# Kernel tuning notes

Hardware: AMD Instinct MI355X
Metric: run time of the kernel (lower is better)

The kernel has to match this reference:

```python
import jax, jax.numpy as jnp
import numpy as np

L, D_IN, D_MODEL, N_LAYERS = 4096, 8, 256, 2
ED, N, K = 512, 16, 4          # d_inner = 2*d_model, d_state, d_conv
DT_RANK = 16                   # ceil(d_model/16)
EPS = 1e-5


def setup_inputs() -> dict:
    key = jax.random.key(0)
    ks = jax.random.split(key, 10)
    def g(k, shape, s=0.02):
        return jax.random.normal(k, shape, jnp.float32) * s
    A_init = jnp.tile(jnp.arange(1, N + 1, dtype=jnp.float32), (N_LAYERS, ED, 1))
    return {
        "x": jax.random.normal(ks[0], (L, D_IN), jnp.float32),
        "fc_in_w": g(ks[1], (D_MODEL, D_IN), 0.1),
        "fc_in_b": jnp.zeros((D_MODEL,), jnp.float32),
        "fc_out_w": g(ks[2], (1, D_MODEL), 0.1),
        "fc_out_b": jnp.zeros((1,), jnp.float32),
        "norm_w": jnp.ones((N_LAYERS, D_MODEL), jnp.float32),
        "in_proj_w": g(ks[3], (N_LAYERS, 2 * ED, D_MODEL)),
        "conv_w": g(ks[4], (N_LAYERS, ED, 1, K), 0.1),
        "conv_b": jnp.zeros((N_LAYERS, ED), jnp.float32),
        "x_proj_w": g(ks[5], (N_LAYERS, DT_RANK + 2 * N, ED)),
        "dt_proj_w": g(ks[6], (N_LAYERS, ED, DT_RANK), 0.1),
        "dt_proj_b": jnp.full((N_LAYERS, ED), -4.0, jnp.float32),  # softplus(-4)~0.018
        "A_log": jnp.log(A_init),
        "D": jnp.ones((N_LAYERS, ED), jnp.float32),
        "out_proj_w": g(ks[7], (N_LAYERS, D_MODEL, ED)),
    }


def rmsnorm(x, w):
    return x * jax.lax.rsqrt(jnp.mean(x * x, axis=-1, keepdims=True) + EPS) * w


def causal_depthwise_conv(x, w, b):
    # x: [L, ED], w: [ED, 1, K] -> causal depthwise conv along L
    y = jax.lax.conv_general_dilated(
        x.T[None],  # [1, ED, L]
        w, (1,), [(K - 1, 0)],
        dimension_numbers=("NCH", "OIH", "NCH"),
        feature_group_count=ED)
    return y[0].T + b  # [L, ED]


def mamba_block(x, p):
    norm_w, in_w, cw, cb, xp_w, dtw, dtb, a_log, d, out_w = p
    xn = rmsnorm(x, norm_w)
    xz = xn @ in_w.T                      # [L, 2*ED]
    xi, z = xz[:, :ED], xz[:, ED:]
    xc = jax.nn.silu(causal_depthwise_conv(xi, cw, cb))   # [L, ED]
    dbc = xc @ xp_w.T                     # [L, DT_RANK + 2N]
    delta = jax.nn.softplus(dbc[:, :DT_RANK] @ dtw.T + dtb)  # [L, ED]
    B = dbc[:, DT_RANK:DT_RANK + N]       # [L, N]
    C = dbc[:, DT_RANK + N:]              # [L, N]
    A = -jnp.exp(a_log)                   # [ED, N]
    dA = jnp.exp(delta[:, :, None] * A[None])                 # [L, ED, N]
    dBx = delta[:, :, None] * B[:, None, :] * xc[:, :, None]  # [L, ED, N]

    def step(h, inp):
        da, dbx, c = inp
        h = da * h + dbx                  # [ED, N]
        return h, jnp.einsum("en,n->e", h, c)

    _, ys = jax.lax.scan(step, jnp.zeros((ED, N), x.dtype), (dA, dBx, C))
    y = (ys + d * xc) * jax.nn.silu(z)
    return x + y @ out_w.T


def forward(x, fc_in_w, fc_in_b, fc_out_w, fc_out_b, norm_w, in_proj_w, conv_w,
            conv_b, x_proj_w, dt_proj_w, dt_proj_b, A_log, D, out_proj_w):
    h = x @ fc_in_w.T + fc_in_b           # [L, D_MODEL]

    def layer(h, p):
        return mamba_block(h, p), None

    h, _ = jax.lax.scan(layer, h, (norm_w, in_proj_w, conv_w, conv_b, x_proj_w,
                                   dt_proj_w, dt_proj_b, A_log, D, out_proj_w))
    out = jnp.tanh(h @ fc_out_w.T + fc_out_b)  # [L, 1]
    return out.reshape(-1)


def reference(x, fc_in_w, fc_in_b, fc_out_w, fc_out_b, norm_w, in_proj_w, conv_w,
              conv_b, x_proj_w, dt_proj_w, dt_proj_b, A_log, D, out_proj_w):
    return forward(x, fc_in_w, fc_in_b, fc_out_w, fc_out_b, norm_w, in_proj_w,
                   conv_w, conv_b, x_proj_w, dt_proj_w, dt_proj_b, A_log, D,
                   out_proj_w)
```

## Files before the change

kernel.cpp:

```cpp
#include <hip/hip_runtime.h>
#include <math.h>

#define LSEQ 4096
#define D_IN 8
#define D_MODEL 256
#define ED 512
#define NSTATE 16
#define KCONV 4
#define DT_RANK 16
#define EPS 1e-5f
#define NCHUNK 256
#define CHUNK 16

typedef short short8 __attribute__((ext_vector_type(8)));
typedef unsigned short ushort8 __attribute__((ext_vector_type(8)));
typedef unsigned short ushort4v __attribute__((ext_vector_type(4)));
typedef float f32x4 __attribute__((ext_vector_type(4)));

__device__ __forceinline__ float sigmoidf_(float x){ return 1.f/(1.f+__expf(-x)); }
__device__ __forceinline__ float siluf_(float x){ return x*sigmoidf_(x); }
__device__ __forceinline__ float softplusf_(float x){
  return (x > 20.f) ? x : log1pf(__expf(x));
}
__device__ __forceinline__ unsigned short f2bf(float f){
  unsigned int u = __float_as_uint(f);
  return (unsigned short)((u + 0x7fffu + ((u>>16)&1u)) >> 16);
}
__device__ __forceinline__ float bf2f(unsigned short u){
  return __uint_as_float(((unsigned int)u) << 16);
}

__global__ void k_prep(const float* __restrict__ x, const float* __restrict__ fiw,
                       const float* __restrict__ fib, const float* __restrict__ ipw,
                       const float* __restrict__ xpw, const float* __restrict__ opw,
                       float* __restrict__ h, unsigned short* __restrict__ wip,
                       unsigned short* __restrict__ wxp, unsigned short* __restrict__ wop){
  int b = blockIdx.x, tid = threadIdx.x;
  if (b < 816) {
    int i4 = b*256 + tid;
    const float* src; unsigned short* dst;
    if (i4 < 131072)      { src = ipw; dst = wip; }
    else if (i4 < 143360) { i4 -= 131072; src = xpw; dst = wxp; }
    else                  { i4 -= 143360; src = opw; dst = wop; }
    float4 v = ((const float4*)src)[i4];
    ushort4v o;
    o.x = f2bf(v.x); o.y = f2bf(v.y); o.z = f2bf(v.z); o.w = f2bf(v.w);
    ((ushort4v*)dst)[i4] = o;
  } else {
    int idx = (b-816)*256 + tid;
    int t = idx >> 8, d = idx & 255;
    float acc = fib[d];
#pragma unroll
    for (int i = 0; i < D_IN; ++i) acc += x[t*D_IN+i]*fiw[d*D_IN+i];
    h[idx] = acc;
  }
}

template<int WM, int WN, bool RMS, bool ACC, bool ABF16, bool CBF16>
__global__ __launch_bounds__(256) void k_gemm_mfma(
    const void* __restrict__ Ap, const unsigned short* __restrict__ B,
    void* __restrict__ Cp, int M, int N, int K, const float* __restrict__ nwp)
{
  constexpr int BM = 32*WM, BN = 32*WN, LDT = 72;
  const float* A = (const float*)Ap;
  const unsigned short* Ab = (const unsigned short*)Ap;
  float* Cf = (float*)Cp;
  unsigned short* Cb = (unsigned short*)Cp;
  __shared__ unsigned short As[BM*LDT];
  __shared__ unsigned short Bs[BN*LDT];
  __shared__ float rms_lds[BM];
  __shared__ float nws[D_MODEL];
  const int tid = threadIdx.x;
  const int bm = blockIdx.x*BM, bn = blockIdx.y*BN;
  const int w = tid >> 6, lane = tid & 63;
  const int mb = (w>>1)*WM*16, nb = (w&1)*WN*16;
  const int lr = lane & 15, lk = (lane>>4)*8;
  if (RMS) {
    nws[tid] = nwp[tid];
    constexpr int TPR = 256/BM;
    constexpr int SEG = D_MODEL/TPR;
    int row = tid / TPR, part = tid % TPR;
    const float* ap = A + (size_t)(bm+row)*K + part*SEG;
    float s = 0.f;
#pragma unroll
    for (int i = 0; i < SEG; i += 4) {
      float4 v = *(const float4*)&ap[i];
      s += v.x*v.x + v.y*v.y + v.z*v.z + v.w*v.w;
    }
#pragma unroll
    for (int m = TPR>>1; m; m >>= 1) s += __shfl_xor(s, m);
    if (part == 0) rms_lds[row] = rsqrtf(s*(1.f/D_MODEL) + EPS);
    __syncthreads();
  }
  f32x4 acc[WM][WN] = {};
  for (int k0 = 0; k0 < K; k0 += 64) {
#pragma unroll 2
    for (int s = tid; s < BM*8; s += 256) {
      int row = s>>3, kg = (s&7)*8;
      if (ABF16) {
        *(ushort8*)&As[row*LDT+kg] = *(const ushort8*)&Ab[(size_t)(bm+row)*K + k0 + kg];
      } else {
        const float* ap = &A[(size_t)(bm+row)*K + k0 + kg];
        float4 a0 = *(const float4*)ap, a1 = *(const float4*)(ap+4);
        if (RMS) {
          float rs = rms_lds[row];
          a0.x *= rs*nws[k0+kg+0]; a0.y *= rs*nws[k0+kg+1];
          a0.z *= rs*nws[k0+kg+2]; a0.w *= rs*nws[k0+kg+3];
          a1.x *= rs*nws[k0+kg+4]; a1.y *= rs*nws[k0+kg+5];
          a1.z *= rs*nws[k0+kg+6]; a1.w *= rs*nws[k0+kg+7];
        }
        ushort8 o;
        o[0]=f2bf(a0.x); o[1]=f2bf(a0.y); o[2]=f2bf(a0.z); o[3]=f2bf(a0.w);
        o[4]=f2bf(a1.x); o[5]=f2bf(a1.y); o[6]=f2bf(a1.z); o[7]=f2bf(a1.w);
        *(ushort8*)&As[row*LDT+kg] = o;
      }
    }
#pragma unroll 2
    for (int s = tid; s < BN*8; s += 256) {
      int row = s>>3, kg = (s&7)*8;
      *(ushort8*)&Bs[row*LDT+kg] = *(const ushort8*)&B[(size_t)(bn+row)*K + k0 + kg];
    }
    __syncthreads();
#pragma unroll
    for (int kk = 0; kk < 2; ++kk) {
      short8 af[WM], bfr[WN];
#pragma unroll
      for (int i = 0; i < WM; ++i) af[i]  = *(const short8*)&As[(mb+i*16+lr)*LDT + kk*32 + lk];
#pragma unroll
      for (int j = 0; j < WN; ++j) bfr[j] = *(const short8*)&Bs[(nb+j*16+lr)*LDT + kk*32 + lk];
#pragma unroll
      for (int i = 0; i < WM; ++i)
#pragma unroll
        for (int j = 0; j < WN; ++j)
          acc[i][j] = __builtin_amdgcn_mfma_f32_16x16x32_bf16(af[i], bfr[j], acc[i][j], 0, 0, 0);
    }
    __syncthreads();
  }
#pragma unroll
  for (int i = 0; i < WM; ++i)
#pragma unroll
    for (int j = 0; j < WN; ++j) {
      int col = bn + nb + j*16 + lr;
#pragma unroll
      for (int r = 0; r < 4; ++r) {
        int row = bm + mb + i*16 + (lane>>4)*4 + r;
        size_t o = (size_t)row*N + col;
        if (CBF16)      Cb[o] = f2bf(acc[i][j][r]);
        else if (ACC)   Cf[o] = Cf[o] + acc[i][j][r];
        else            Cf[o] = acc[i][j][r];
      }
    }
}

__global__ __launch_bounds__(512) void k_cxps1(
    const unsigned short* __restrict__ xzb, const float* __restrict__ cw,
    const float* __restrict__ cb, const unsigned short* __restrict__ wxp,
    const float* __restrict__ dtw, const float* __restrict__ dtb,
    const float* __restrict__ alog, float* __restrict__ dbc,
    float* __restrict__ S, unsigned short* __restrict__ Q)
{
  constexpr int LDA = ED + 8;
  __shared__ unsigned short As[CHUNK*LDA];
  __shared__ float Ds[CHUNK][DT_RANK];
  __shared__ float Bsh[CHUNK][NSTATE];
  const int tid = threadIdx.x;
  const int e = tid;
  const int c = blockIdx.x;
  const int t0 = c*CHUNK;
  float cwv[KCONV];
#pragma unroll
  for (int k = 0; k < KCONV; ++k) cwv[k] = cw[e*KCONV+k];
  float cbv = cb[e];
  float w0=0.f, w1=0.f, w2=0.f;
  if (t0 > 0) {
    w0 = bf2f(xzb[(size_t)(t0-3)*(2*ED) + e]);
    w1 = bf2f(xzb[(size_t)(t0-2)*(2*ED) + e]);
    w2 = bf2f(xzb[(size_t)(t0-1)*(2*ED) + e]);
  }
  float xv[CHUNK];
#pragma unroll
  for (int t = 0; t < CHUNK; ++t) {
    float cur = bf2f(xzb[(size_t)(t0+t)*(2*ED) + e]);
    float v = siluf_(cbv + w0*cwv[0] + w1*cwv[1] + w2*cwv[2] + cur*cwv[3]);
    xv[t] = v;
    w0=w1; w1=w2; w2=cur;
  }
#pragma unroll
  for (int t = 0; t < CHUNK; ++t) {
    unsigned int us = f2bf(xv[t]);
    unsigned int other = (unsigned int)__shfl_down((int)us, 1);
    if ((tid & 1) == 0) *(unsigned int*)&As[t*LDA + e] = us | (other << 16);
  }
  __syncthreads();
  const int w = tid >> 6, lane = tid & 63;
  const int lr = lane & 15, lk = (lane>>4)*8;
  if (w < 3) {
    f32x4 acc = {};
#pragma unroll
    for (int ks = 0; ks < ED/32; ++ks) {
      short8 af = *(const short8*)&As[lr*LDA + ks*32 + lk];
      short8 bf = *(const short8*)&wxp[(size_t)(w*16+lr)*ED + ks*32 + lk];
      acc = __builtin_amdgcn_mfma_f32_16x16x32_bf16(af, bf, acc, 0, 0, 0);
    }
#pragma unroll
    for (int r = 0; r < 4; ++r) {
      int row = (lane>>4)*4 + r;
      dbc[(size_t)(t0+row)*48 + w*16 + lr] = acc[r];
      if (w == 0) Ds[row][lr] = acc[r];
      else if (w == 1) Bsh[row][lr] = acc[r];
    }
  }
  __syncthreads();
  float dtwv[DT_RANK];
#pragma unroll
  for (int r = 0; r < DT_RANK; ++r) dtwv[r] = dtw[e*DT_RANK+r];
  float dtbv = dtb[e];
  float A[NSTATE], h[NSTATE];
#pragma unroll
  for (int n = 0; n < NSTATE; ++n) { A[n] = -__expf(alog[e*NSTATE+n]); h[n] = 0.f; }
  float sd = 0.f;
#pragma unroll
  for (int t = 0; t < CHUNK; ++t) {
    float da = dtbv;
#pragma unroll
    for (int r = 0; r < DT_RANK; ++r) da += Ds[t][r]*dtwv[r];
    float d = softplusf_(da);
    sd += d;
    float dx = d*xv[t];
#pragma unroll
    for (int n = 0; n < NSTATE; ++n)
      h[n] = __expf(d*A[n])*h[n] + dx*Bsh[t][n];
  }
  S[(size_t)c*ED + e] = sd;
#pragma unroll
  for (int n = 0; n < NSTATE; ++n) Q[(size_t)(c*NSTATE+n)*ED + e] = f2bf(h[n]);
}

__global__ __launch_bounds__(512) void k_scan2(
    const float* __restrict__ alog, const float* __restrict__ S,
    unsigned short* __restrict__ Q)
{
  constexpr int NSEG = 16, STEPS = NCHUNK/NSEG;
  __shared__ float Pl[NSEG][32], Rl[NSEG][32], Hs[NSEG][32];
  const int tid = threadIdx.x;
  const int seg = tid >> 5, chl = tid & 31;
  const int ch = blockIdx.x*32 + chl;
  const int n = ch >> 9, e = ch & 511;
  const float a = -__expf(alog[e*NSTATE+n]);
  const int c0 = seg*STEPS;
  float ev[STEPS], qv[STEPS];
#pragma unroll
  for (int k = 0; k < STEPS; ++k) ev[k] = S[(size_t)(c0+k)*ED + e];
#pragma unroll
  for (int k = 0; k < STEPS; ++k) qv[k] = bf2f(Q[(size_t)((c0+k)*NSTATE+n)*ED + e]);
#pragma unroll
  for (int k = 0; k < STEPS; ++k) ev[k] = __expf(a*ev[k]);
  float P = 1.f, R = 0.f;
#pragma unroll
  for (int k = 0; k < STEPS; ++k) { R = ev[k]*R + qv[k]; P *= ev[k]; }
  Pl[seg][chl] = P; Rl[seg][chl] = R;
  __syncthreads();
  if (tid < 32) {
    float hcur = 0.f;
#pragma unroll
    for (int s = 0; s < NSEG; ++s) { Hs[s][tid] = hcur; hcur = Pl[s][tid]*hcur + Rl[s][tid]; }
  }
  __syncthreads();
  float h = Hs[seg][chl];
#pragma unroll
  for (int k = 0; k < STEPS; ++k) {
    float hl = qv[k];
    Q[(size_t)((c0+k)*NSTATE+n)*ED + e] = f2bf(h);
    h = ev[k]*h + hl;
  }
}

__global__ __launch_bounds__(512) void k_scan3(
    const unsigned short* __restrict__ xzb, const float* __restrict__ dbc,
    const float* __restrict__ cw, const float* __restrict__ cb,
    const float* __restrict__ dtw, const float* __restrict__ dtb,
    const float* __restrict__ alog, const unsigned short* __restrict__ Hin,
    const float* __restrict__ Dv, unsigned short* __restrict__ y)
{
  __shared__ float Ds[CHUNK][DT_RANK];
  __shared__ float Bsh[CHUNK][NSTATE];
  __shared__ float Cs[CHUNK][NSTATE];
  const int tid = threadIdx.x;
  const int e = tid;
  const int c = blockIdx.x;
  const int t0 = c*CHUNK;
  for (int i = tid; i < CHUNK*48; i += 512) {
    int t = i/48, col = i - t*48;
    float v = dbc[(size_t)(t0+t)*48 + col];
    if (col < DT_RANK) Ds[t][col] = v;
    else if (col < DT_RANK+NSTATE) Bsh[t][col-DT_RANK] = v;
    else Cs[t][col-DT_RANK-NSTATE] = v;
  }
  float cwv[KCONV];
#pragma unroll
  for (int k = 0; k < KCONV; ++k) cwv[k] = cw[e*KCONV+k];
  float cbv = cb[e];
  float w0=0.f, w1=0.f, w2=0.f;
  if (t0 > 0) {
    w0 = bf2f(xzb[(size_t)(t0-3)*(2*ED) + e]);
    w1 = bf2f(xzb[(size_t)(t0-2)*(2*ED) + e]);
    w2 = bf2f(xzb[(size_t)(t0-1)*(2*ED) + e]);
  }
  float x[CHUNK], z[CHUNK];
#pragma unroll
  for (int t = 0; t < CHUNK; ++t) {
    float cur = bf2f(xzb[(size_t)(t0+t)*(2*ED) + e]);
    x[t] = siluf_(cbv + w0*cwv[0] + w1*cwv[1] + w2*cwv[2] + cur*cwv[3]);
    w0=w1; w1=w2; w2=cur;
  }
#pragma unroll
  for (int t = 0; t < CHUNK; ++t) z[t] = bf2f(xzb[(size_t)(t0+t)*(2*ED) + ED + e]);
  __syncthreads();
  float dtwv[DT_RANK];
#pragma unroll
  for (int r = 0; r < DT_RANK; ++r) dtwv[r] = dtw[e*DT_RANK+r];
  float dtbv = dtb[e];
  float A[NSTATE], h[NSTATE];
#pragma unroll
  for (int n = 0; n < NSTATE; ++n) {
    A[n] = -__expf(alog[e*NSTATE+n]);
    h[n] = bf2f(Hin[(size_t)(c*NSTATE+n)*ED + e]);
  }
  float dv = Dv[e];
#pragma unroll
  for (int t = 0; t < CHUNK; ++t) {
    float da = dtbv;
#pragma unroll
    for (int r = 0; r < DT_RANK; ++r) da += Ds[t][r]*dtwv[r];
    float d = softplusf_(da);
    float dx = d*x[t];
    float ysum = 0.f;
#pragma unroll
    for (int n = 0; n < NSTATE; ++n) {
      h[n] = __expf(d*A[n])*h[n] + dx*Bsh[t][n];
      ysum += h[n]*Cs[t][n];
    }
    y[(size_t)(t0+t)*ED + e] = f2bf((ysum + dv*x[t]) * siluf_(z[t]));
  }
}

__global__ void k_fc_out(const float* __restrict__ h, const float* __restrict__ w,
                         const float* __restrict__ b, float* __restrict__ out){
  int wave = threadIdx.x >> 6, lane = threadIdx.x & 63;
  int row = blockIdx.x*4 + wave;
  const float4 hv = *(const float4*)&h[row*D_MODEL + lane*4];
  const float4 wv = *(const float4*)&w[lane*4];
  float s = hv.x*wv.x + hv.y*wv.y + hv.z*wv.z + hv.w*wv.w;
#pragma unroll
  for (int m = 32; m; m >>= 1) s += __shfl_xor(s, m);
  if (lane == 0) out[row] = tanhf(s + b[0]);
}

extern "C" void kernel_launch(void* const* d_in, const int* in_sizes, int n_in,
                              void* d_out, int out_size, void* d_ws, size_t ws_size,
                              hipStream_t stream){
  const float* x    = (const float*)d_in[0];
  const float* fiw  = (const float*)d_in[1];
  const float* fib  = (const float*)d_in[2];
  const float* fow  = (const float*)d_in[3];
  const float* fob  = (const float*)d_in[4];
  const float* nw   = (const float*)d_in[5];
  const float* ipw  = (const float*)d_in[6];
  const float* cw   = (const float*)d_in[7];
  const float* cb   = (const float*)d_in[8];
  const float* xpw  = (const float*)d_in[9];
  const float* dtw  = (const float*)d_in[10];
  const float* dtb  = (const float*)d_in[11];
  const float* alog = (const float*)d_in[12];
  const float* Dv   = (const float*)d_in[13];
  const float* opw  = (const float*)d_in[14];

  float* W = (float*)d_ws;
  float* h   = W;
  float* dbc = h   + (size_t)LSEQ*D_MODEL;
  float* S   = dbc + (size_t)LSEQ*48;
  unsigned short* xzb = (unsigned short*)(S + (size_t)NCHUNK*ED);
  unsigned short* Q   = xzb + (size_t)LSEQ*2*ED;
  unsigned short* yb  = Q   + (size_t)NCHUNK*NSTATE*ED;
  unsigned short* wip = yb  + (size_t)LSEQ*ED;
  unsigned short* wxp = wip + (size_t)2*2*ED*D_MODEL;
  unsigned short* wop = wxp + (size_t)2*48*ED;

  k_prep<<<816 + LSEQ, 256, 0, stream>>>(x, fiw, fib, ipw, xpw, opw, h, wip, wxp, wop);

  for (int l = 0; l < 2; ++l) {
    const unsigned short* wip_l = wip + (size_t)l*2*ED*D_MODEL;
    const unsigned short* wxp_l = wxp + (size_t)l*48*ED;
    const unsigned short* wop_l = wop + (size_t)l*D_MODEL*ED;
    const float* nw_l   = nw   + l*D_MODEL;
    const float* cw_l   = cw   + l*ED*KCONV;
    const float* cb_l   = cb   + l*ED;
    const float* dtw_l  = dtw  + l*ED*DT_RANK;
    const float* dtb_l  = dtb  + l*ED;
    const float* alog_l = alog + l*ED*NSTATE;
    const float* D_l    = Dv   + l*ED;

    k_gemm_mfma<2,2,true,false,false,true><<<dim3(LSEQ/64, (2*ED)/64), 256, 0, stream>>>(
        h, wip_l, xzb, LSEQ, 2*ED, D_MODEL, nw_l);
    k_cxps1<<<NCHUNK, 512, 0, stream>>>(xzb, cw_l, cb_l, wxp_l, dtw_l, dtb_l, alog_l,
                                        dbc, S, Q);
    k_scan2<<<NCHUNK, 512, 0, stream>>>(alog_l, S, Q);
    k_scan3<<<NCHUNK, 512, 0, stream>>>(xzb, dbc, cw_l, cb_l, dtw_l, dtb_l, alog_l,
                                        Q, D_l, yb);
    k_gemm_mfma<1,1,false,true,true,false><<<dim3(LSEQ/32, D_MODEL/32), 256, 0, stream>>>(
        yb, wop_l, h, LSEQ, D_MODEL, ED, nullptr);
  }

  k_fc_out<<<LSEQ/4, 256, 0, stream>>>(h, fow, fob, (float*)d_out);
}
```

Baseline: 171.4 us.

## Halve scan chunk size to double chunk-level parallelism and restructure fc_in prep

Shrinks the chunked selective-scan chunk from 16 to 8 timesteps, doubling the number of chunk blocks in the conv/xproj pass and the output pass so more CUs are busy. The cross-chunk scan is rebalanced to 16 channels by 32 segments per block, and the MFMA x_proj tile masks out the unused upper rows. The fc_in part of the prep kernel now computes 8 timesteps per block, reusing weights held in registers and inputs staged in shared memory, instead of one output per thread. The cost is a longer inter-chunk carry scan, more Q/S traffic, and half-wasted 16-row MFMA tiles.

```diff
diff --git a/kernel.cpp b/kernel.cpp
--- a/kernel.cpp
+++ b/kernel.cpp
@@ -9,8 +9,8 @@
 #define KCONV 4
 #define DT_RANK 16
 #define EPS 1e-5f
-#define NCHUNK 256
-#define CHUNK 16
+#define NCHUNK 512
+#define CHUNK 8
 
 typedef short short8 __attribute__((ext_vector_type(8)));
 typedef unsigned short ushort8 __attribute__((ext_vector_type(8)));
@@ -35,6 +35,7 @@
                        const float* __restrict__ xpw, const float* __restrict__ opw,
                        float* __restrict__ h, unsigned short* __restrict__ wip,
                        unsigned short* __restrict__ wxp, unsigned short* __restrict__ wop){
+  __shared__ float xs[64];
   int b = blockIdx.x, tid = threadIdx.x;
   if (b < 816) {
     int i4 = b*256 + tid;
@@ -47,12 +48,20 @@
     o.x = f2bf(v.x); o.y = f2bf(v.y); o.z = f2bf(v.z); o.w = f2bf(v.w);
     ((ushort4v*)dst)[i4] = o;
   } else {
-    int idx = (b-816)*256 + tid;
-    int t = idx >> 8, d = idx & 255;
-    float acc = fib[d];
-#pragma unroll
-    for (int i = 0; i < D_IN; ++i) acc += x[t*D_IN+i]*fiw[d*D_IN+i];
-    h[idx] = acc;
+    int t0 = (b-816)*8;
+    if (tid < 64) xs[tid] = x[t0*D_IN + tid];
+    __syncthreads();
+    int d = tid;
+    const float4 wa = *(const float4*)&fiw[d*D_IN];
+    const float4 wb = *(const float4*)&fiw[d*D_IN+4];
+    float bv = fib[d];
+#pragma unroll
+    for (int t = 0; t < 8; ++t) {
+      float acc = bv
+        + xs[t*8+0]*wa.x + xs[t*8+1]*wa.y + xs[t*8+2]*wa.z + xs[t*8+3]*wa.w
+        + xs[t*8+4]*wb.x + xs[t*8+5]*wb.y + xs[t*8+6]*wb.z + xs[t*8+7]*wb.w;
+      h[(size_t)(t0+t)*D_MODEL + d] = acc;
+    }
   }
 }
 
@@ -160,7 +169,7 @@
     float* __restrict__ S, unsigned short* __restrict__ Q)
 {
   constexpr int LDA = ED + 8;
-  __shared__ unsigned short As[CHUNK*LDA];
+  __shared__ unsigned short As[16*LDA];
   __shared__ float Ds[CHUNK][DT_RANK];
   __shared__ float Bsh[CHUNK][NSTATE];
   const int tid = threadIdx.x;
@@ -205,9 +214,11 @@
 #pragma unroll
     for (int r = 0; r < 4; ++r) {
       int row = (lane>>4)*4 + r;
-      dbc[(size_t)(t0+row)*48 + w*16 + lr] = acc[r];
-      if (w == 0) Ds[row][lr] = acc[r];
-      else if (w == 1) Bsh[row][lr] = acc[r];
+      if (row < CHUNK) {
+        dbc[(size_t)(t0+row)*48 + w*16 + lr] = acc[r];
+        if (w == 0) Ds[row][lr] = acc[r];
+        else if (w == 1) Bsh[row][lr] = acc[r];
+      }
     }
   }
   __syncthreads();
@@ -240,11 +251,11 @@
     const float* __restrict__ alog, const float* __restrict__ S,
     unsigned short* __restrict__ Q)
 {
-  constexpr int NSEG = 16, STEPS = NCHUNK/NSEG;
-  __shared__ float Pl[NSEG][32], Rl[NSEG][32], Hs[NSEG][32];
+  constexpr int NSEG = 32, STEPS = NCHUNK/NSEG;
+  __shared__ float Pl[NSEG][16], Rl[NSEG][16], Hs[NSEG][16];
   const int tid = threadIdx.x;
-  const int seg = tid >> 5, chl = tid & 31;
-  const int ch = blockIdx.x*32 + chl;
+  const int seg = tid >> 4, chl = tid & 15;
+  const int ch = blockIdx.x*16 + chl;
   const int n = ch >> 9, e = ch & 511;
   const float a = -__expf(alog[e*NSTATE+n]);
   const int c0 = seg*STEPS;
@@ -260,7 +271,7 @@
   for (int k = 0; k < STEPS; ++k) { R = ev[k]*R + qv[k]; P *= ev[k]; }
   Pl[seg][chl] = P; Rl[seg][chl] = R;
   __syncthreads();
-  if (tid < 32) {
+  if (tid < 16) {
     float hcur = 0.f;
 #pragma unroll
     for (int s = 0; s < NSEG; ++s) { Hs[s][tid] = hcur; hcur = Pl[s][tid]*hcur + Rl[s][tid]; }
@@ -289,8 +300,8 @@
   const int e = tid;
   const int c = blockIdx.x;
   const int t0 = c*CHUNK;
-  for (int i = tid; i < CHUNK*48; i += 512) {
-    int t = i/48, col = i - t*48;
+  if (tid < CHUNK*48) {
+    int t = tid/48, col = tid - t*48;
     float v = dbc[(size_t)(t0+t)*48 + col];
     if (col < DT_RANK) Ds[t][col] = v;
     else if (col < DT_RANK+NSTATE) Bsh[t][col-DT_RANK] = v;
@@ -386,7 +397,7 @@
   unsigned short* wxp = wip + (size_t)2*2*ED*D_MODEL;
   unsigned short* wop = wxp + (size_t)2*48*ED;
 
-  k_prep<<<816 + LSEQ, 256, 0, stream>>>(x, fiw, fib, ipw, xpw, opw, h, wip, wxp, wop);
+  k_prep<<<816 + LSEQ/8, 256, 0, stream>>>(x, fiw, fib, ipw, xpw, opw, h, wip, wxp, wop);
 
   for (int l = 0; l < 2; ++l) {
     const unsigned short* wip_l = wip + (size_t)l*2*ED*D_MODEL;
@@ -404,7 +415,7 @@
         h, wip_l, xzb, LSEQ, 2*ED, D_MODEL, nw_l);
     k_cxps1<<<NCHUNK, 512, 0, stream>>>(xzb, cw_l, cb_l, wxp_l, dtw_l, dtb_l, alog_l,
                                         dbc, S, Q);
-    k_scan2<<<NCHUNK, 512, 0, stream>>>(alog_l, S, Q);
+    k_scan2<<<ED*NSTATE/16, 512, 0, stream>>>(alog_l, S, Q);
     k_scan3<<<NCHUNK, 512, 0, stream>>>(xzb, dbc, cw_l, cb_l, dtw_l, dtb_l, alog_l,
                                         Q, D_l, yb);
     k_gemm_mfma<1,1,false,true,true,false><<<dim3(LSEQ/32, D_MODEL/32), 256, 0, stream>>>(
```

Result: slower. 182.5 us (+6.5%).
